# Performance work log

Measured on AMD Instinct MI355X. Metric: run time of the kernel, lower is better.

## Reference

```python
import jax, jax.numpy as jnp
import numpy as np
from jax import lax

EOS_TOKEN = 2
VOCAB = 32000
EMB = 256
HID = 512
BATCH = 64
SEQ = 1024
N_EOS = 32  # EOS tokens per sequence (fixed so output shape is deterministic)


def setup_inputs() -> dict:
    key = jax.random.key(0)
    k_tok, k_pos, k_emb, k_wi, k_wh, k_bi, k_bh = jax.random.split(key, 7)
    # tokens in [3, VOCAB) so EOS only appears where we place it
    tokens = jax.random.randint(k_tok, (BATCH, SEQ), 3, VOCAB)
    # place exactly N_EOS EOS tokens per row at sorted random positions
    perms = jax.vmap(lambda k: jax.random.permutation(k, SEQ))(
        jax.random.split(k_pos, BATCH))
    eos_pos = jnp.sort(perms[:, :N_EOS], axis=1)  # [B, N_EOS]
    rows = jnp.arange(BATCH)[:, None]
    tokens = tokens.at[rows, eos_pos].set(EOS_TOKEN)
    s = 1.0 / np.sqrt(HID)
    return {
        "input_tokens": tokens.astype(jnp.int64) if jax.config.jax_enable_x64 else tokens.astype(jnp.int32),
        "emb_table": jax.random.normal(k_emb, (VOCAB, EMB), jnp.float32),
        "w_ih": jax.random.uniform(k_wi, (3 * HID, EMB), jnp.float32, -s, s),
        "w_hh": jax.random.uniform(k_wh, (3 * HID, HID), jnp.float32, -s, s),
        "b_ih": jax.random.uniform(k_bi, (3 * HID,), jnp.float32, -s, s),
        "b_hh": jax.random.uniform(k_bh, (3 * HID,), jnp.float32, -s, s),
    }


def _gru(embedded, w_ih, w_hh, b_ih, b_hh):
    # embedded: [S, B, E]; PyTorch GRU cell math, h0 = 0
    S, B, _ = embedded.shape
    H = w_hh.shape[1]
    # precompute input projections for all timesteps: [S, B, 3H]
    gi_all = jnp.einsum('sbe,ge->sbg', embedded, w_ih) + b_ih

    def step(h, gi):
        gh = h @ w_hh.T + b_hh                      # [B, 3H]
        i_r, i_z, i_n = jnp.split(gi, 3, axis=-1)
        h_r, h_z, h_n = jnp.split(gh, 3, axis=-1)
        r = jax.nn.sigmoid(i_r + h_r)
        z = jax.nn.sigmoid(i_z + h_z)
        n = jnp.tanh(i_n + r * h_n)
        h_new = (1.0 - z) * n + z * h
        return h_new, h_new

    h0 = jnp.zeros((B, H), embedded.dtype)
    _, outs = lax.scan(step, h0, gi_all)           # outs: [S, B, H]
    return outs


def reference(input_tokens, emb_table, w_ih, w_hh, b_ih, b_hh):
    tokens_t = input_tokens.T                       # [S, B]
    embedded = emb_table[tokens_t]                  # [S, B, E]
    outputs = _gru(embedded, w_ih, w_hh, b_ih, b_hh)  # [S, B, H]

    mask = tokens_t == EOS_TOKEN                    # [S, B]
    counts = mask.sum(0)
    C = int(np.max(np.asarray(counts)))             # deterministic = N_EOS by construction
    # compaction: k-th EOS output of column b goes to c[k, b]
    dest = jnp.where(mask, jnp.cumsum(mask, axis=0) - 1, C)  # [S, B]; C = dump row
    B, H = outputs.shape[1], outputs.shape[2]
    c = jnp.zeros((C + 1, B, H), outputs.dtype)
    c = c.at[dest, jnp.arange(B)[None, :]].add(jnp.where(mask[..., None], outputs, 0.0))
    return c[:C]
```

## Files before the change

### kernel.cpp

```cpp
#include <hip/hip_runtime.h>
#include <hip/hip_bf16.h>

typedef __attribute__((ext_vector_type(8))) short  bf16x8;
typedef __attribute__((ext_vector_type(4))) float  f32x4;
typedef __attribute__((ext_vector_type(4))) unsigned int u32x4;

#define EOS 2
#define S 1024
#define B 64
#define E 256
#define H 512

#define CNT_SLOTS 1032
#define CNT_STRIDE 4
#define HBUF_OFF 131072
#define DEST_OFF 655360
#define MEMSET_BYTES 655360

#define AT_LD(p)    __hip_atomic_load((p), __ATOMIC_RELAXED, __HIP_MEMORY_SCOPE_AGENT)
#define AT_ST(p, v) __hip_atomic_store((p), (v), __ATOMIC_RELAXED, __HIP_MEMORY_SCOPE_AGENT)
#define AT_ADD(p,v) __hip_atomic_fetch_add((p), (v), __ATOMIC_RELAXED, __HIP_MEMORY_SCOPE_AGENT)

__device__ __forceinline__ unsigned short f2bf(float f) {
    unsigned int u = __builtin_bit_cast(unsigned int, f);
    unsigned int r = (u + 0x7FFFu + ((u >> 16) & 1u)) >> 16;
    return (unsigned short)r;
}
__device__ __forceinline__ float bf2f(unsigned short s) {
    unsigned int u = ((unsigned int)s) << 16;
    return __builtin_bit_cast(float, u);
}
__device__ __forceinline__ unsigned int pk2(float x, float y) {
    unsigned int ux = __builtin_bit_cast(unsigned int, x) + 0x8000u;
    unsigned int uy = __builtin_bit_cast(unsigned int, y) + 0x8000u;
    return (ux >> 16) | (uy & 0xFFFF0000u);
}
__device__ __forceinline__ bf16x8 pack8hu(float4 a, float4 b) {
    union { unsigned int d[4]; bf16x8 v; } u;
    u.d[0] = pk2(a.x, a.y); u.d[1] = pk2(a.z, a.w);
    u.d[2] = pk2(b.x, b.y); u.d[3] = pk2(b.z, b.w);
    return u.v;
}
__device__ __forceinline__ bf16x8 pack8rne(float4 a, float4 b) {
    union { unsigned short s[8]; bf16x8 v; } u;
    u.s[0] = f2bf(a.x); u.s[1] = f2bf(a.y); u.s[2] = f2bf(a.z); u.s[3] = f2bf(a.w);
    u.s[4] = f2bf(b.x); u.s[5] = f2bf(b.y); u.s[6] = f2bf(b.z); u.s[7] = f2bf(b.w);
    return u.v;
}

__global__ __launch_bounds__(256) void dest_kernel(const int* __restrict__ tokens,
                                                   signed char* __restrict__ dest8) {
    const int b = blockIdx.x, tid = threadIdx.x;
    const int l = tid & 63, w = tid >> 6;
    const int base = tid * 4;
    int m[4], cnt = 0;
#pragma unroll
    for (int i = 0; i < 4; ++i) {
        int tok = tokens[b * S + base + i];
        m[i] = (tok == EOS) ? 1 : 0;
        cnt += m[i];
    }
    int inc = cnt;
#pragma unroll
    for (int d = 1; d < 64; d <<= 1) {
        int v = __shfl_up(inc, d, 64);
        if (l >= d) inc += v;
    }
    __shared__ int wt[4];
    if (l == 63) wt[w] = inc;
    __syncthreads();
    int off = 0;
    for (int k = 0; k < 4; ++k)
        if (k < w) off += wt[k];
    int run = off + inc - cnt;
#pragma unroll
    for (int i = 0; i < 4; ++i) {
        dest8[(base + i) * B + b] = m[i] ? (signed char)run : (signed char)-1;
        run += m[i];
    }
}

__global__ __launch_bounds__(256, 1) void gru_kernel(
    const int* __restrict__ tokens, const float* __restrict__ emb,
    const float* __restrict__ w_ih, const float* __restrict__ w_hh,
    const float* __restrict__ b_ih, const float* __restrict__ b_hh,
    const signed char* __restrict__ dest8,
    char* ws, float* __restrict__ out) {

    const int tid = threadIdx.x;
    const int wv = tid >> 6;
    const int l = tid & 63;
    const int l15 = l & 15, quad = l >> 4;
    const int blk = blockIdx.x;
    const int w = blk & 3;
    const int j4 = blk >> 2;
    const int unit = (j4 * 4 + wv) * 16 + l15;
    const int koff = quad * 8;
    const int brow = w * 16 + l15;

    unsigned int*   cnt  = (unsigned int*)ws;
    unsigned short* hbuf = (unsigned short*)(ws + HBUF_OFF);

    __shared__ alignas(16) unsigned short sh[2][16][520];

    bf16x8 Wh[3][16];
#pragma unroll
    for (int g = 0; g < 3; ++g)
#pragma unroll
        for (int kt = 0; kt < 16; ++kt) {
            const float* p = &w_hh[(size_t)(g * H + unit) * H + kt * 32 + koff];
            Wh[g][kt] = pack8rne(*(const float4*)p, *(const float4*)(p + 4));
        }
    bf16x8 Wi[3][8];
#pragma unroll
    for (int g = 0; g < 3; ++g)
#pragma unroll
        for (int kt = 0; kt < 8; ++kt) {
            const float* p = &w_ih[(size_t)(g * H + unit) * E + kt * 32 + koff];
            Wi[g][kt] = pack8rne(*(const float4*)p, *(const float4*)(p + 4));
        }
    const float bi0 = b_ih[unit], bi1 = b_ih[H + unit], bi2 = b_ih[2 * H + unit];
    const float bh0 = b_hh[unit], bh1 = b_hh[H + unit], bh2 = b_hh[2 * H + unit];

    float hown[4] = {0.f, 0.f, 0.f, 0.f};
    int tok_next = tokens[brow * S];
    int budget = 1 << 22;

    const int p_st  = tid >> 7;
    const int rr_st = (tid >> 3) & 15;
    const int t7    = tid & 7;

    for (int t = 0; t < S; ++t) {
        const int tok = tok_next;
        const float* er = &emb[(size_t)tok * E + koff];
        float4 ef[8][2];
#pragma unroll
        for (int kt = 0; kt < 8; ++kt) {
            ef[kt][0] = *(const float4*)(er + kt * 32);
            ef[kt][1] = *(const float4*)(er + kt * 32 + 4);
        }
        if (t + 1 < S) tok_next = tokens[brow * S + t + 1];
        unsigned int dword =
            *(const unsigned int*)&dest8[t * B + w * 16 + quad * 4];

        f32x4 gi0 = {bi0, bi0, bi0, bi0};
        f32x4 gi1 = {bi1, bi1, bi1, bi1};
        f32x4 gi2 = {bi2, bi2, bi2, bi2};
#pragma unroll
        for (int kt = 0; kt < 8; ++kt) {
            bf16x8 af = pack8hu(ef[kt][0], ef[kt][1]);
            gi0 = __builtin_amdgcn_mfma_f32_16x16x32_bf16(af, Wi[0][kt], gi0, 0, 0, 0);
            gi1 = __builtin_amdgcn_mfma_f32_16x16x32_bf16(af, Wi[1][kt], gi1, 0, 0, 0);
            gi2 = __builtin_amdgcn_mfma_f32_16x16x32_bf16(af, Wi[2][kt], gi2, 0, 0, 0);
        }

        if (t > 0) {
            const unsigned int* cp =
                &cnt[((unsigned)w * CNT_SLOTS + (unsigned)t) * CNT_STRIDE];
            while (budget > 0) {
                unsigned int c = AT_LD(cp);
                if (c >= 8u) break;
                --budget;
            }
        }

        {
            const unsigned short* hs = hbuf + (size_t)(t & 1) * (2 * B * H);
            const unsigned short* gp =
                hs + (size_t)p_st * (B * H) + (size_t)(w * 16 + rr_st) * H + t7 * 8;
            u32x4 gr[8];
            asm volatile(
                "global_load_dwordx4 %0, %8, off sc1\n\t"
                "global_load_dwordx4 %1, %8, off offset:128 sc1\n\t"
                "global_load_dwordx4 %2, %8, off offset:256 sc1\n\t"
                "global_load_dwordx4 %3, %8, off offset:384 sc1\n\t"
                "global_load_dwordx4 %4, %8, off offset:512 sc1\n\t"
                "global_load_dwordx4 %5, %8, off offset:640 sc1\n\t"
                "global_load_dwordx4 %6, %8, off offset:768 sc1\n\t"
                "global_load_dwordx4 %7, %8, off offset:896 sc1\n\t"
                "s_waitcnt vmcnt(0)"
                : "=&v"(gr[0]), "=&v"(gr[1]), "=&v"(gr[2]), "=&v"(gr[3]),
                  "=&v"(gr[4]), "=&v"(gr[5]), "=&v"(gr[6]), "=&v"(gr[7])
                : "v"(gp)
                : "memory");
#pragma unroll
            for (int c = 0; c < 8; ++c)
                *(u32x4*)&sh[p_st][rr_st][t7 * 8 + c * 64] = gr[c];
        }
        __syncthreads();

        f32x4 a0 = {bh0, bh0, bh0, bh0};
        f32x4 a1 = {bh1, bh1, bh1, bh1};
        f32x4 a2 = {bh2, bh2, bh2, bh2};
#pragma unroll
        for (int kt = 0; kt < 16; ++kt) {
            bf16x8 ah = *(const bf16x8*)&sh[0][l15][kt * 32 + koff];
            bf16x8 al = *(const bf16x8*)&sh[1][l15][kt * 32 + koff];
            a0 = __builtin_amdgcn_mfma_f32_16x16x32_bf16(ah, Wh[0][kt], a0, 0, 0, 0);
            a1 = __builtin_amdgcn_mfma_f32_16x16x32_bf16(ah, Wh[1][kt], a1, 0, 0, 0);
            a2 = __builtin_amdgcn_mfma_f32_16x16x32_bf16(ah, Wh[2][kt], a2, 0, 0, 0);
            a0 = __builtin_amdgcn_mfma_f32_16x16x32_bf16(al, Wh[0][kt], a0, 0, 0, 0);
            a1 = __builtin_amdgcn_mfma_f32_16x16x32_bf16(al, Wh[1][kt], a1, 0, 0, 0);
            a2 = __builtin_amdgcn_mfma_f32_16x16x32_bf16(al, Wh[2][kt], a2, 0, 0, 0);
        }

        unsigned short* hd = hbuf + (size_t)((t + 1) & 1) * (2 * B * H);
        unsigned int* hd_hi32 = (unsigned int*)hd;
        unsigned int* hd_lo32 = (unsigned int*)(hd + B * H);
        const bool even = (l15 & 1) == 0;
#pragma unroll
        for (int r = 0; r < 4; ++r) {
            const int b = w * 16 + quad * 4 + r;
            float rg = 1.f / (1.f + __expf(-(gi0[r] + a0[r])));
            float zg = 1.f / (1.f + __expf(-(gi1[r] + a1[r])));
            float x = gi2[r] + rg * a2[r];
            x = fminf(15.f, fmaxf(-15.f, x));
            float e = __expf(-2.f * x);
            float ng = (1.f - e) / (1.f + e);
            float h = (1.f - zg) * ng + zg * hown[r];
            hown[r] = h;
            unsigned short hi16 = f2bf(h);
            unsigned short lo16 = f2bf(h - bf2f(hi16));
            unsigned int pk = ((unsigned int)lo16 << 16) | (unsigned int)hi16;
            unsigned int sw = (unsigned int)__shfl_xor((int)pk, 1);
            unsigned int val = even ? ((pk & 0xFFFFu) | (sw << 16))
                                    : ((sw >> 16) | (pk & 0xFFFF0000u));
            unsigned int didx = ((unsigned int)(b * H + unit)) >> 1;
            AT_ST((even ? hd_hi32 : hd_lo32) + didx, val);
        }

        asm volatile("s_waitcnt vmcnt(0)" ::: "memory");
        __syncthreads();
        if (tid == 0)
            AT_ADD(&cnt[((unsigned)w * CNT_SLOTS + (unsigned)(t + 1)) * CNT_STRIDE], 1u);

#pragma unroll
        for (int r = 0; r < 4; ++r) {
            const int b = w * 16 + quad * 4 + r;
            int db = (int)(signed char)((dword >> (8 * r)) & 0xFFu);
            if (db >= 0)
                out[((size_t)(db * B + b)) * H + unit] = hown[r];
        }
    }
}

extern "C" void kernel_launch(void* const* d_in, const int* in_sizes, int n_in,
                              void* d_out, int out_size, void* d_ws, size_t ws_size,
                              hipStream_t stream) {
    const int*   tokens = (const int*)d_in[0];
    const float* emb    = (const float*)d_in[1];
    const float* w_ih   = (const float*)d_in[2];
    const float* w_hh   = (const float*)d_in[3];
    const float* b_ih   = (const float*)d_in[4];
    const float* b_hh   = (const float*)d_in[5];
    float* out = (float*)d_out;

    char* ws = (char*)d_ws;
    signed char* dest8 = (signed char*)(ws + DEST_OFF);

    hipMemsetAsync(d_ws, 0, MEMSET_BYTES, stream);
    dest_kernel<<<B, 256, 0, stream>>>(tokens, dest8);
    gru_kernel<<<32, 256, 0, stream>>>(tokens, emb, w_ih, w_hh, b_ih, b_hh,
                                       dest8, ws, out);
}
```

Measured before the change: 5.558 ms.

## Replace counter-based inter-block barrier with sentinel-polled hidden-state ring buffer

Drops the per-step atomic counter that blocks polled before reading the shared hidden state. Blocks now read the bf16 hidden state directly and retry until no sentinel (0xFFFFFFFF) words remain. The state lives in a 4-slot ring, and each block writes sentinels back into its portion of the slot two steps ahead. This takes a global atomic add and a separate poll round trip off the serial per-timestep critical path. It also adds an XOR swizzle to the LDS layout in place of padding, to avoid bank conflicts. The risks are that a legitimate hi/lo bf16 pair could equal the sentinel, and that correctness depends on the reset writes being ordered correctly relative to readers.

```diff
diff --git a/kernel.cpp b/kernel.cpp
--- a/kernel.cpp
+++ b/kernel.cpp
@@ -10,16 +10,13 @@
 #define B 64
 #define E 256
 #define H 512
-
-#define CNT_SLOTS 1032
-#define CNT_STRIDE 4
-#define HBUF_OFF 131072
-#define DEST_OFF 655360
-#define MEMSET_BYTES 655360
-
-#define AT_LD(p)    __hip_atomic_load((p), __ATOMIC_RELAXED, __HIP_MEMORY_SCOPE_AGENT)
+#define SENT 0xFFFFFFFFu
+
+#define HBUF_OFF 4096
+#define SLOT (2 * B * H)
+#define DEST_OFF (HBUF_OFF + 4 * SLOT * 2)
+
 #define AT_ST(p, v) __hip_atomic_store((p), (v), __ATOMIC_RELAXED, __HIP_MEMORY_SCOPE_AGENT)
-#define AT_ADD(p,v) __hip_atomic_fetch_add((p), (v), __ATOMIC_RELAXED, __HIP_MEMORY_SCOPE_AGENT)
 
 __device__ __forceinline__ unsigned short f2bf(float f) {
     unsigned int u = __builtin_bit_cast(unsigned int, f);
@@ -98,10 +95,9 @@
     const int koff = quad * 8;
     const int brow = w * 16 + l15;
 
-    unsigned int*   cnt  = (unsigned int*)ws;
     unsigned short* hbuf = (unsigned short*)(ws + HBUF_OFF);
 
-    __shared__ alignas(16) unsigned short sh[2][16][520];
+    __shared__ alignas(16) unsigned short sh[2][16][512];
 
     bf16x8 Wh[3][16];
 #pragma unroll
@@ -124,7 +120,7 @@
 
     float hown[4] = {0.f, 0.f, 0.f, 0.f};
     int tok_next = tokens[brow * S];
-    int budget = 1 << 22;
+    int budget = 1 << 21;
 
     const int p_st  = tid >> 7;
     const int rr_st = (tid >> 3) & 15;
@@ -154,38 +150,47 @@
             gi2 = __builtin_amdgcn_mfma_f32_16x16x32_bf16(af, Wi[2][kt], gi2, 0, 0, 0);
         }
 
-        if (t > 0) {
-            const unsigned int* cp =
-                &cnt[((unsigned)w * CNT_SLOTS + (unsigned)t) * CNT_STRIDE];
-            while (budget > 0) {
-                unsigned int c = AT_LD(cp);
-                if (c >= 8u) break;
-                --budget;
-            }
-        }
-
         {
-            const unsigned short* hs = hbuf + (size_t)(t & 1) * (2 * B * H);
+            const unsigned short* hs = hbuf + (size_t)(t & 3) * SLOT;
             const unsigned short* gp =
                 hs + (size_t)p_st * (B * H) + (size_t)(w * 16 + rr_st) * H + t7 * 8;
             u32x4 gr[8];
-            asm volatile(
-                "global_load_dwordx4 %0, %8, off sc1\n\t"
-                "global_load_dwordx4 %1, %8, off offset:128 sc1\n\t"
-                "global_load_dwordx4 %2, %8, off offset:256 sc1\n\t"
-                "global_load_dwordx4 %3, %8, off offset:384 sc1\n\t"
-                "global_load_dwordx4 %4, %8, off offset:512 sc1\n\t"
-                "global_load_dwordx4 %5, %8, off offset:640 sc1\n\t"
-                "global_load_dwordx4 %6, %8, off offset:768 sc1\n\t"
-                "global_load_dwordx4 %7, %8, off offset:896 sc1\n\t"
-                "s_waitcnt vmcnt(0)"
-                : "=&v"(gr[0]), "=&v"(gr[1]), "=&v"(gr[2]), "=&v"(gr[3]),
-                  "=&v"(gr[4]), "=&v"(gr[5]), "=&v"(gr[6]), "=&v"(gr[7])
-                : "v"(gp)
-                : "memory");
-#pragma unroll
-            for (int c = 0; c < 8; ++c)
-                *(u32x4*)&sh[p_st][rr_st][t7 * 8 + c * 64] = gr[c];
+            unsigned int bad;
+            do {
+                asm volatile(
+                    "global_load_dwordx4 %0, %8, off sc1\n\t"
+                    "global_load_dwordx4 %1, %8, off offset:128 sc1\n\t"
+                    "global_load_dwordx4 %2, %8, off offset:256 sc1\n\t"
+                    "global_load_dwordx4 %3, %8, off offset:384 sc1\n\t"
+                    "global_load_dwordx4 %4, %8, off offset:512 sc1\n\t"
+                    "global_load_dwordx4 %5, %8, off offset:640 sc1\n\t"
+                    "global_load_dwordx4 %6, %8, off offset:768 sc1\n\t"
+                    "global_load_dwordx4 %7, %8, off offset:896 sc1\n\t"
+                    "s_waitcnt vmcnt(0)"
+                    : "=&v"(gr[0]), "=&v"(gr[1]), "=&v"(gr[2]), "=&v"(gr[3]),
+                      "=&v"(gr[4]), "=&v"(gr[5]), "=&v"(gr[6]), "=&v"(gr[7])
+                    : "v"(gp)
+                    : "memory");
+                bad = 0;
+#pragma unroll
+                for (int c = 0; c < 8; ++c)
+                    bad |= (unsigned)((gr[c][0] == SENT) | (gr[c][1] == SENT) |
+                                      (gr[c][2] == SENT) | (gr[c][3] == SENT));
+            } while (bad && --budget > 0);
+#pragma unroll
+            for (int c = 0; c < 8; ++c) {
+                int pos = ((t7 + 8 * c) ^ (rr_st & 7)) * 8;
+                *(u32x4*)&sh[p_st][rr_st][pos] = gr[c];
+            }
+        }
+
+        {
+            unsigned short* rs = hbuf + (size_t)((t + 2) & 3) * SLOT;
+            const size_t rbase = (size_t)(w * 16 + (tid >> 4)) * H + j4 * 64;
+            unsigned int* ph = (unsigned int*)(rs + rbase) + (tid & 15) * 2;
+            unsigned int* pl = (unsigned int*)(rs + B * H + rbase) + (tid & 15) * 2;
+            AT_ST(ph, SENT); AT_ST(ph + 1, SENT);
+            AT_ST(pl, SENT); AT_ST(pl + 1, SENT);
         }
         __syncthreads();
 
@@ -194,8 +199,9 @@
         f32x4 a2 = {bh2, bh2, bh2, bh2};
 #pragma unroll
         for (int kt = 0; kt < 16; ++kt) {
-            bf16x8 ah = *(const bf16x8*)&sh[0][l15][kt * 32 + koff];
-            bf16x8 al = *(const bf16x8*)&sh[1][l15][kt * 32 + koff];
+            const int pos = ((kt * 4 + quad) ^ (l15 & 7)) * 8;
+            bf16x8 ah = *(const bf16x8*)&sh[0][l15][pos];
+            bf16x8 al = *(const bf16x8*)&sh[1][l15][pos];
             a0 = __builtin_amdgcn_mfma_f32_16x16x32_bf16(ah, Wh[0][kt], a0, 0, 0, 0);
             a1 = __builtin_amdgcn_mfma_f32_16x16x32_bf16(ah, Wh[1][kt], a1, 0, 0, 0);
             a2 = __builtin_amdgcn_mfma_f32_16x16x32_bf16(ah, Wh[2][kt], a2, 0, 0, 0);
@@ -204,13 +210,10 @@
             a2 = __builtin_amdgcn_mfma_f32_16x16x32_bf16(al, Wh[2][kt], a2, 0, 0, 0);
         }
 
-        unsigned short* hd = hbuf + (size_t)((t + 1) & 1) * (2 * B * H);
-        unsigned int* hd_hi32 = (unsigned int*)hd;
-        unsigned int* hd_lo32 = (unsigned int*)(hd + B * H);
-        const bool even = (l15 & 1) == 0;
+        float hval[4];
+        unsigned int pkv[4];
 #pragma unroll
         for (int r = 0; r < 4; ++r) {
-            const int b = w * 16 + quad * 4 + r;
             float rg = 1.f / (1.f + __expf(-(gi0[r] + a0[r])));
             float zg = 1.f / (1.f + __expf(-(gi1[r] + a1[r])));
             float x = gi2[r] + rg * a2[r];
@@ -218,28 +221,36 @@
             float e = __expf(-2.f * x);
             float ng = (1.f - e) / (1.f + e);
             float h = (1.f - zg) * ng + zg * hown[r];
-            hown[r] = h;
+            hown[r] = h; hval[r] = h;
             unsigned short hi16 = f2bf(h);
             unsigned short lo16 = f2bf(h - bf2f(hi16));
-            unsigned int pk = ((unsigned int)lo16 << 16) | (unsigned int)hi16;
-            unsigned int sw = (unsigned int)__shfl_xor((int)pk, 1);
-            unsigned int val = even ? ((pk & 0xFFFFu) | (sw << 16))
-                                    : ((sw >> 16) | (pk & 0xFFFF0000u));
-            unsigned int didx = ((unsigned int)(b * H + unit)) >> 1;
-            AT_ST((even ? hd_hi32 : hd_lo32) + didx, val);
+            pkv[r] = ((unsigned int)lo16 << 16) | (unsigned int)hi16;
         }
 
         asm volatile("s_waitcnt vmcnt(0)" ::: "memory");
+        {
+            unsigned short* hd = hbuf + (size_t)((t + 1) & 3) * SLOT;
+            unsigned int* hd_hi32 = (unsigned int*)hd;
+            unsigned int* hd_lo32 = (unsigned int*)(hd + B * H);
+            const bool even = (l15 & 1) == 0;
+#pragma unroll
+            for (int r = 0; r < 4; ++r) {
+                const int b = w * 16 + quad * 4 + r;
+                unsigned int sw = (unsigned int)__shfl_xor((int)pkv[r], 1);
+                unsigned int val = even ? ((pkv[r] & 0xFFFFu) | (sw << 16))
+                                        : ((sw >> 16) | (pkv[r] & 0xFFFF0000u));
+                unsigned int didx = ((unsigned int)(b * H + unit)) >> 1;
+                AT_ST((even ? hd_hi32 : hd_lo32) + didx, val);
+            }
+        }
         __syncthreads();
-        if (tid == 0)
-            AT_ADD(&cnt[((unsigned)w * CNT_SLOTS + (unsigned)(t + 1)) * CNT_STRIDE], 1u);
 
 #pragma unroll
         for (int r = 0; r < 4; ++r) {
             const int b = w * 16 + quad * 4 + r;
             int db = (int)(signed char)((dword >> (8 * r)) & 0xFFu);
             if (db >= 0)
-                out[((size_t)(db * B + b)) * H + unit] = hown[r];
+                out[((size_t)(db * B + b)) * H + unit] = hval[r];
         }
     }
 }
@@ -258,7 +269,8 @@
     char* ws = (char*)d_ws;
     signed char* dest8 = (signed char*)(ws + DEST_OFF);
 
-    hipMemsetAsync(d_ws, 0, MEMSET_BYTES, stream);
+    hipMemsetAsync(ws + HBUF_OFF, 0, SLOT * 2, stream);
+    hipMemsetAsync(ws + HBUF_OFF + SLOT * 2, 0xFF, 3 * SLOT * 2, stream);
     dest_kernel<<<B, 256, 0, stream>>>(tokens, dest8);
     gru_kernel<<<32, 256, 0, stream>>>(tokens, emb, w_ih, w_hh, b_ih, b_hh,
                                        dest8, ws, out);
```

New measurement: 5.385 ms. 3.1% less time.
